# Kernel tuning notes

Measured on AMD Instinct MI355X. Metric: run time of the kernel, lower is better.

Reference implementation:

```python
import jax, jax.numpy as jnp
import numpy as np

N = 50000        # nodes
E = 800000       # edges
F_IN = 128       # num_node_features
H = 128          # hidden_size
C = 128          # num_classes (must be 128 for lin1 to typecheck)
G = 64           # graphs in batch


def setup_inputs() -> dict:
    key = jax.random.key(0)
    ks = jax.random.split(key, 12)
    x = jax.random.normal(ks[0], (N, F_IN), dtype=jnp.float32)
    edge_index = jax.random.randint(ks[1], (2, E), 0, N, dtype=jnp.int64)
    batch = jnp.sort(jax.random.randint(ks[2], (N,), 0, G, dtype=jnp.int64))

    def glorot(k, i, o):
        return jax.random.normal(k, (i, o), dtype=jnp.float32) / np.float32(np.sqrt(i))

    return {
        'x': x, 'edge_index': edge_index, 'batch': batch,
        'W1': glorot(ks[3], F_IN, H), 'b1': jnp.zeros((H,), jnp.float32),
        'W2': glorot(ks[4], H, H),    'b2': jnp.zeros((H,), jnp.float32),
        'W3': glorot(ks[5], H, C),    'b3': jnp.zeros((C,), jnp.float32),
        'Wl': glorot(ks[6], 128, C),  'bl': jnp.zeros((C,), jnp.float32),
    }


def _gcn_conv(x, W, b, src, dst, n):
    # PyG GCNConv: h = x W; out_i = sum_{j->i} d_j^-1/2 d_i^-1/2 h_j + b
    h = x @ W                                                   # [n, out]
    deg = jax.ops.segment_sum(jnp.ones(dst.shape[0], h.dtype), dst, num_segments=n)
    dinv = jnp.where(deg > 0, jax.lax.rsqrt(jnp.maximum(deg, 1.0)), 0.0)
    norm = dinv[src] * dinv[dst]                                # [E+n]
    msg = h[src] * norm[:, None]                                # gather + scale
    return jax.ops.segment_sum(msg, dst, num_segments=n) + b    # scatter-add


def reference(x, edge_index, batch, W1, b1, W2, b2, W3, b3, Wl, bl):
    x = x.astype(jnp.float32)
    loops = jnp.arange(N, dtype=edge_index.dtype)
    src = jnp.concatenate([edge_index[0], loops])  # add self-loops
    dst = jnp.concatenate([edge_index[1], loops])

    h = jax.nn.elu(_gcn_conv(x, W1, b1, src, dst, N))
    h = jax.nn.elu(_gcn_conv(h, W2, b2, src, dst, N))
    h = jax.nn.elu(_gcn_conv(h, W3, b3, src, dst, N))

    # global_mean_pool over batch vector
    cnt = jax.ops.segment_sum(jnp.ones(N, h.dtype), batch, num_segments=G)
    pooled = jax.ops.segment_sum(h, batch, num_segments=G) / jnp.maximum(cnt, 1.0)[:, None]

    # dropout(p=0.2) is identity in eval mode
    return pooled @ Wl + bl
```

## Files before the change

kernel.cpp:

```cpp
#include <hip/hip_runtime.h>
#include <hip/hip_bf16.h>
#include <hip/hip_fp16.h>

#define N_NODES 50000
#define N_GRAPHS 64
#define FILL_CHUNK 4096
#define SLOTS 64
#define SLOT_SHIFT 6
#define PSHIFT 7
#define NPARTS ((N_NODES + 127) >> 7)
#define MM_BLOCKS ((N_NODES + 63) / 64)

typedef _Float16 f16x8 __attribute__((ext_vector_type(8)));
typedef float f32x4 __attribute__((ext_vector_type(4)));


__device__ inline unsigned short f2h_bits(float x) {
    _Float16 h = (_Float16)x;
    return __builtin_bit_cast(unsigned short, h);
}
__device__ inline float h_bits2f(unsigned short b) {
    return (float)__builtin_bit_cast(_Float16, b);
}
__device__ inline unsigned pack_h2(float a, float b) {
    return (unsigned)f2h_bits(a) | ((unsigned)f2h_bits(b) << 16);
}

__device__ inline void fma_h8(float (&acc)[8], uint4 v, float w) {
    acc[0] += w * h_bits2f((unsigned short)(v.x & 0xffffu));
    acc[1] += w * h_bits2f((unsigned short)(v.x >> 16));
    acc[2] += w * h_bits2f((unsigned short)(v.y & 0xffffu));
    acc[3] += w * h_bits2f((unsigned short)(v.y >> 16));
    acc[4] += w * h_bits2f((unsigned short)(v.z & 0xffffu));
    acc[5] += w * h_bits2f((unsigned short)(v.z >> 16));
    acc[6] += w * h_bits2f((unsigned short)(v.w & 0xffffu));
    acc[7] += w * h_bits2f((unsigned short)(v.w >> 16));
}

template<typename BUCKET>
__device__ inline void agg_loop(const uint4* __restrict__ hb4, BUCKET bucket, int n8,
                                int li, float (&acc)[8]) {
    uint4 c0 = make_uint4(0, 0, 0, 0), c1 = c0;
    if (n8 > 0) { c0 = bucket[0]; c1 = bucket[1]; }
    for (int e8 = 0; e8 < n8; ++e8) {
        uint4 nx0 = make_uint4(0, 0, 0, 0), nx1 = nx0;
        if (e8 + 1 < n8) { nx0 = bucket[2 * e8 + 2]; nx1 = bucket[2 * e8 + 3]; }
        uint4 v0 = hb4[(size_t)(c0.x >> 16) * 16 + li];
        uint4 v1 = hb4[(size_t)(c0.y >> 16) * 16 + li];
        uint4 v2 = hb4[(size_t)(c0.z >> 16) * 16 + li];
        uint4 v3 = hb4[(size_t)(c0.w >> 16) * 16 + li];
        uint4 v4 = hb4[(size_t)(c1.x >> 16) * 16 + li];
        uint4 v5 = hb4[(size_t)(c1.y >> 16) * 16 + li];
        uint4 v6 = hb4[(size_t)(c1.z >> 16) * 16 + li];
        uint4 v7 = hb4[(size_t)(c1.w >> 16) * 16 + li];
        fma_h8(acc, v0, h_bits2f((unsigned short)(c0.x & 0xffffu)));
        fma_h8(acc, v1, h_bits2f((unsigned short)(c0.y & 0xffffu)));
        fma_h8(acc, v2, h_bits2f((unsigned short)(c0.z & 0xffffu)));
        fma_h8(acc, v3, h_bits2f((unsigned short)(c0.w & 0xffffu)));
        fma_h8(acc, v4, h_bits2f((unsigned short)(c1.x & 0xffffu)));
        fma_h8(acc, v5, h_bits2f((unsigned short)(c1.y & 0xffffu)));
        fma_h8(acc, v6, h_bits2f((unsigned short)(c1.z & 0xffffu)));
        fma_h8(acc, v7, h_bits2f((unsigned short)(c1.w & 0xffffu)));
        c0 = nx0; c1 = nx1;
    }
}

__device__ inline void bias_elu(const float* __restrict__ bias, float di, int li,
                                float (&acc)[8], float (&o)[8]) {
    float4 b0 = *(const float4*)&bias[li * 8];
    float4 b1 = *(const float4*)&bias[li * 8 + 4];
    o[0] = di * acc[0] + b0.x; o[1] = di * acc[1] + b0.y;
    o[2] = di * acc[2] + b0.z; o[3] = di * acc[3] + b0.w;
    o[4] = di * acc[4] + b1.x; o[5] = di * acc[5] + b1.y;
    o[6] = di * acc[6] + b1.z; o[7] = di * acc[7] + b1.w;
    #pragma unroll
    for (int i = 0; i < 8; ++i) o[i] = o[i] > 0.f ? o[i] : expm1f(o[i]);
}

__device__ inline void aggregate_node(const uint4* __restrict__ hb4,
                                      const int* __restrict__ deg,
                                      const uint4* __restrict__ cvp4,
                                      const float* __restrict__ dinv,
                                      const float* __restrict__ bias,
                                      int node, int li, float (&o)[8]) {
    int dg = min(deg[node], SLOTS);
    int n8 = (dg + 7) >> 3;
    const uint4* bucket = cvp4 + ((size_t)node << (SLOT_SHIFT - 2));
    float di = dinv[node];

    float acc[8];
    #pragma unroll
    for (int i = 0; i < 8; ++i) acc[i] = 0.f;
    uint4 h = hb4[(size_t)node * 16 + li];
    fma_h8(acc, h, di);
    agg_loop(hb4, bucket, n8, li, acc);
    bias_elu(bias, di, li, acc, o);
}


__global__ __launch_bounds__(256) void prep_kernel(const int* __restrict__ dst,
                                                   int* __restrict__ cntmat,
                                                   const float* __restrict__ W1,
                                                   const float* __restrict__ W2,
                                                   const float* __restrict__ W3,
                                                   unsigned short* __restrict__ Wt,
                                                   float* __restrict__ pooled,
                                                   int ne, int nch) {
    int blk = blockIdx.x;
    if (blk < nch) {
        __shared__ int h[NPARTS];
        for (int i = threadIdx.x; i < NPARTS; i += 256) h[i] = 0;
        __syncthreads();
        int beg = blk * FILL_CHUNK, end = min(beg + FILL_CHUNK, ne);
        for (int i = beg + threadIdx.x; i < end; i += 256)
            atomicAdd(&h[dst[i] >> PSHIFT], 1);
        __syncthreads();
        for (int i = threadIdx.x; i < NPARTS; i += 256) cntmat[blk * NPARTS + i] = h[i];
    } else if (blk < nch + 192) {
        int i = (blk - nch) * 256 + threadIdx.x;
        int which = i >> 14;
        const float* W = (which == 0) ? W1 : (which == 1) ? W2 : W3;
        int j = i & 16383;
        int nn = j >> 7, k = j & 127;
        Wt[(which << 14) + nn * 128 + k] = f2h_bits(W[k * 128 + nn]);
    } else {
        int i = (blk - nch - 192) * 256 + threadIdx.x;
        if (i < N_GRAPHS * 128) pooled[i] = 0.f;
    }
}


__global__ __launch_bounds__(256) void scanp_mm_kernel(int* __restrict__ cntmat,
                                                       int* __restrict__ ptotal, int nchunks,
                                                       const float* __restrict__ x,
                                                       const unsigned short* __restrict__ Wt,
                                                       unsigned short* __restrict__ Hh, int n) {
    __shared__ unsigned short Wl[128 * 136];
    int blk = blockIdx.x;
    int t = threadIdx.x;

    if (blk < NPARTS) {
        int* s = (int*)Wl;
        int p = blk;
        int v = (t < nchunks) ? cntmat[t * NPARTS + p] : 0;
        s[t] = v;
        __syncthreads();
        #pragma unroll
        for (int d = 1; d < 256; d <<= 1) {
            int y = (t >= d) ? s[t - d] : 0;
            __syncthreads();
            s[t] += y;
            __syncthreads();
        }
        if (t < nchunks) cntmat[t * NPARTS + p] = s[t] - v;
        if (t == 255) ptotal[p] = s[255];
        return;
    }

    {
        int row = t >> 1, seg = t & 1;
        #pragma unroll
        for (int j = 0; j < 8; ++j) {
            int c = seg * 64 + j * 8;
            *(uint4*)&Wl[row * 136 + c] = *(const uint4*)&Wt[row * 128 + c];
        }
    }
    __syncthreads();

    int w = t >> 6, lane = t & 63;
    int lm = lane & 15, lg = lane >> 4;
    int r0 = (blk - NPARTS) * 64 + w * 16;

    f32x4 acc[8];
    #pragma unroll
    for (int ct = 0; ct < 8; ++ct) acc[ct] = (f32x4){0.f, 0.f, 0.f, 0.f};

    int ar = min(r0 + lm, n - 1);

    #pragma unroll
    for (int kk = 0; kk < 4; ++kk) {
        const float* arow = x + (size_t)ar * 128;
        float4 lo = *(const float4*)&arow[kk * 32 + lg * 8];
        float4 hi = *(const float4*)&arow[kk * 32 + lg * 8 + 4];
        f16x8 a;
        a[0] = (_Float16)lo.x; a[1] = (_Float16)lo.y;
        a[2] = (_Float16)lo.z; a[3] = (_Float16)lo.w;
        a[4] = (_Float16)hi.x; a[5] = (_Float16)hi.y;
        a[6] = (_Float16)hi.z; a[7] = (_Float16)hi.w;
        #pragma unroll
        for (int ct = 0; ct < 8; ++ct) {
            f16x8 b = *(const f16x8*)&Wl[(ct * 16 + lm) * 136 + kk * 32 + lg * 8];
            acc[ct] = __builtin_amdgcn_mfma_f32_16x16x32_f16(a, b, acc[ct], 0, 0, 0);
        }
    }

    #pragma unroll
    for (int ct = 0; ct < 8; ++ct) {
        #pragma unroll
        for (int i = 0; i < 4; ++i) {
            int rr = r0 + lg * 4 + i;
            if (rr < n) Hh[(size_t)rr * 128 + ct * 16 + lm] = f2h_bits(acc[ct][i]);
        }
    }
}

__global__ __launch_bounds__(512) void scant_kernel(const int* __restrict__ ptotal,
                                                    int* __restrict__ pbase) {
    __shared__ int s[512];
    int t = threadIdx.x;
    int v = (t < NPARTS) ? ptotal[t] : 0;
    s[t] = v;
    __syncthreads();
    #pragma unroll
    for (int d = 1; d < 512; d <<= 1) {
        int y = (t >= d) ? s[t - d] : 0;
        __syncthreads();
        s[t] += y;
        __syncthreads();
    }
    if (t < NPARTS) pbase[t] = s[t] - v;
    if (t == NPARTS - 1) pbase[NPARTS] = s[t];
}

__global__ __launch_bounds__(256) void bin_scatter_kernel(const int* __restrict__ src,
                                                          const int* __restrict__ dst,
                                                          const int* __restrict__ cntmat,
                                                          const int* __restrict__ pbase,
                                                          unsigned* __restrict__ binned, int ne) {
    __shared__ int pos[NPARTS];
    int c = blockIdx.x, t = threadIdx.x;
    for (int i = t; i < NPARTS; i += 256) pos[i] = pbase[i] + cntmat[c * NPARTS + i];
    __syncthreads();
    int beg = c * FILL_CHUNK, end = min(beg + FILL_CHUNK, ne);
    for (int i = beg + t; i < end; i += 256) {
        int d = dst[i];
        int p = d >> PSHIFT;
        int idx = atomicAdd(&pos[p], 1);
        binned[idx] = ((unsigned)(d & 127) << 16) | (unsigned)src[i];
    }
}

__global__ __launch_bounds__(256) void bucket_fill_kernel(const unsigned* __restrict__ binned,
                                                          const int* __restrict__ pbase,
                                                          int* __restrict__ deg,
                                                          float* __restrict__ dinv,
                                                          unsigned* __restrict__ tag,
                                                          uint4* __restrict__ cvp4, int n) {
    __shared__ unsigned bkt[128 * SLOTS];
    __shared__ int curls[128];
    int p = blockIdx.x, t = threadIdx.x;
    if (t < 128) curls[t] = 0;
    __syncthreads();
    int beg = pbase[p], end = pbase[p + 1];
    for (int i = beg + t; i < end; i += 256) {
        unsigned e = binned[i];
        int dl = (int)(e >> 16);
        int ps = atomicAdd(&curls[dl], 1);
        if (ps < SLOTS) bkt[(dl << SLOT_SHIFT) + ps] = e & 0xFFFFu;
    }
    __syncthreads();
    int node0 = p << PSHIFT;
    if (t < 128 && node0 + t < n) {
        int c = curls[t];
        deg[node0 + t] = c;
        float dv = rsqrtf((float)c + 1.0f);
        dinv[node0 + t] = dv;
        tag[node0 + t] = ((unsigned)(node0 + t) << 16) | (unsigned)f2h_bits(dv);
    }
    __syncthreads();
    const uint4* b4 = (const uint4*)bkt;
    uint4* outp = cvp4 + (size_t)p * (128 * SLOTS / 4);
    for (int i = t; i < 128 * (SLOTS / 4); i += 256) {
        int r = i >> 4, s4 = i & 15;
        int lim4 = ((min(curls[r], SLOTS) + 7) & ~7) >> 2;
        if (s4 < lim4) outp[i] = b4[i];
    }
}


__global__ __launch_bounds__(256) void fused_tag_agg_mm_kernel(const uint4* __restrict__ hb4,
                                                               const int* __restrict__ deg,
                                                               const unsigned* __restrict__ tag,
                                                               uint4* __restrict__ cvp4,
                                                               const float* __restrict__ dinv,
                                                               const float* __restrict__ bias,
                                                               const unsigned short* __restrict__ Wt,
                                                               unsigned short* __restrict__ Hh,
                                                               int n) {
    __shared__ uint4 bkt4[16 * 16];
    __shared__ unsigned short actl[16 * 136];
    int t = threadIdx.x;
    int nl = t >> 4;
    int li = t & 15;
    int node = blockIdx.x * 16 + nl;

    {
        int slot0 = li << 2;
        int dgn = min(deg[node], SLOTS);
        int lim = (dgn + 7) & ~7;
        uint4 r = make_uint4(0, 0, 0, 0);
        if (slot0 < lim) {
            uint4 v = cvp4[(size_t)node * 16 + li];
            r.x = (slot0     < dgn) ? tag[v.x & 0xFFFFu] : 0u;
            r.y = (slot0 + 1 < dgn) ? tag[v.y & 0xFFFFu] : 0u;
            r.z = (slot0 + 2 < dgn) ? tag[v.z & 0xFFFFu] : 0u;
            r.w = (slot0 + 3 < dgn) ? tag[v.w & 0xFFFFu] : 0u;
            cvp4[(size_t)node * 16 + li] = r;
        }
        bkt4[nl * 16 + li] = r;
    }
    __syncthreads();

    int dg = min(deg[node], SLOTS);
    int n8 = (dg + 7) >> 3;
    float di = dinv[node];

    float acc[8];
    #pragma unroll
    for (int i = 0; i < 8; ++i) acc[i] = 0.f;
    uint4 h = hb4[(size_t)node * 16 + li];
    fma_h8(acc, h, di);
    agg_loop(hb4, (const uint4*)&bkt4[nl * 16], n8, li, acc);

    float o[8];
    bias_elu(bias, di, li, acc, o);

    uint4 pk;
    pk.x = pack_h2(o[0], o[1]);
    pk.y = pack_h2(o[2], o[3]);
    pk.z = pack_h2(o[4], o[5]);
    pk.w = pack_h2(o[6], o[7]);
    *(uint4*)&actl[nl * 136 + li * 8] = pk;

    __syncthreads();

    int w = t >> 6, lane = t & 63;
    int lm = lane & 15, lg = lane >> 4;

    f32x4 macc[2];
    macc[0] = (f32x4){0.f, 0.f, 0.f, 0.f};
    macc[1] = (f32x4){0.f, 0.f, 0.f, 0.f};

    #pragma unroll
    for (int kk = 0; kk < 4; ++kk) {
        f16x8 a = *(const f16x8*)&actl[lm * 136 + kk * 32 + lg * 8];
        #pragma unroll
        for (int j = 0; j < 2; ++j) {
            int ct = w * 2 + j;
            f16x8 b = *(const f16x8*)&Wt[(size_t)(ct * 16 + lm) * 128 + kk * 32 + lg * 8];
            macc[j] = __builtin_amdgcn_mfma_f32_16x16x32_f16(a, b, macc[j], 0, 0, 0);
        }
    }

    #pragma unroll
    for (int j = 0; j < 2; ++j) {
        int ct = w * 2 + j;
        #pragma unroll
        for (int i = 0; i < 4; ++i) {
            int rr = blockIdx.x * 16 + lg * 4 + i;
            Hh[(size_t)rr * 128 + ct * 16 + lm] = f2h_bits(macc[j][i]);
        }
    }
}


__global__ __launch_bounds__(256) void fused_agg_mm_kernel(const uint4* __restrict__ hb4,
                                                           const int* __restrict__ deg,
                                                           const uint4* __restrict__ cvp4,
                                                           const float* __restrict__ dinv,
                                                           const float* __restrict__ bias,
                                                           const unsigned short* __restrict__ Wt,
                                                           unsigned short* __restrict__ Hh,
                                                           int n) {
    __shared__ unsigned short Wl[128 * 136];
    __shared__ unsigned short actl[16 * 136];
    int t = threadIdx.x;

    {
        int row = t >> 1, seg = t & 1;
        #pragma unroll
        for (int j = 0; j < 8; ++j) {
            int c = seg * 64 + j * 8;
            *(uint4*)&Wl[row * 136 + c] = *(const uint4*)&Wt[row * 128 + c];
        }
    }

    int nl = t >> 4;
    int li = t & 15;
    int node = blockIdx.x * 16 + nl;

    float o[8];
    aggregate_node(hb4, deg, cvp4, dinv, bias, node, li, o);

    uint4 pk;
    pk.x = pack_h2(o[0], o[1]);
    pk.y = pack_h2(o[2], o[3]);
    pk.z = pack_h2(o[4], o[5]);
    pk.w = pack_h2(o[6], o[7]);
    *(uint4*)&actl[nl * 136 + li * 8] = pk;

    __syncthreads();

    int w = t >> 6, lane = t & 63;
    int lm = lane & 15, lg = lane >> 4;

    f32x4 macc[2];
    macc[0] = (f32x4){0.f, 0.f, 0.f, 0.f};
    macc[1] = (f32x4){0.f, 0.f, 0.f, 0.f};

    #pragma unroll
    for (int kk = 0; kk < 4; ++kk) {
        f16x8 a = *(const f16x8*)&actl[lm * 136 + kk * 32 + lg * 8];
        #pragma unroll
        for (int j = 0; j < 2; ++j) {
            int ct = w * 2 + j;
            f16x8 b = *(const f16x8*)&Wl[(ct * 16 + lm) * 136 + kk * 32 + lg * 8];
            macc[j] = __builtin_amdgcn_mfma_f32_16x16x32_f16(a, b, macc[j], 0, 0, 0);
        }
    }

    #pragma unroll
    for (int j = 0; j < 2; ++j) {
        int ct = w * 2 + j;
        #pragma unroll
        for (int i = 0; i < 4; ++i) {
            int rr = blockIdx.x * 16 + lg * 4 + i;
            Hh[(size_t)rr * 128 + ct * 16 + lm] = f2h_bits(macc[j][i]);
        }
    }
}


__global__ __launch_bounds__(256) void fused_agg_pool_kernel(const uint4* __restrict__ hb4,
                                                             const int* __restrict__ deg,
                                                             const uint4* __restrict__ cvp4,
                                                             const float* __restrict__ dinv,
                                                             const float* __restrict__ bias,
                                                             const int* __restrict__ batch,
                                                             float* __restrict__ pooled,
                                                             int n) {
    __shared__ float plds[16][132];
    __shared__ int gid[16];
    int t = threadIdx.x;
    int nl = t >> 4;
    int li = t & 15;
    int node = blockIdx.x * 16 + nl;

    if (t < 16) gid[t] = batch[blockIdx.x * 16 + t];

    float o[8];
    aggregate_node(hb4, deg, cvp4, dinv, bias, node, li, o);

    #pragma unroll
    for (int i = 0; i < 8; ++i) plds[nl][li * 8 + i] = o[i];

    __syncthreads();

    int f = t & 127, rg = t >> 7;
    int r0 = rg * 8;
    float local = 0.f;
    int gprev = gid[r0];
    #pragma unroll
    for (int r = r0; r < r0 + 8; ++r) {
        int g = gid[r];
        if (g != gprev) {
            atomicAdd(&pooled[gprev * 128 + f], local);
            local = 0.f;
            gprev = g;
        }
        local += plds[r][f];
    }
    atomicAdd(&pooled[gprev * 128 + f], local);
}


__global__ __launch_bounds__(128) void linear_kernel(const float* __restrict__ pooled,
                                                     const int* __restrict__ batch,
                                                     const float* __restrict__ Wl,
                                                     const float* __restrict__ bl,
                                                     float* __restrict__ out, int n) {
    __shared__ float p[128];
    int g = blockIdx.x, t = threadIdx.x;

    int lo = 0, hi = n;
    while (lo < hi) { int m = (lo + hi) >> 1; if (batch[m] < g) lo = m + 1; else hi = m; }
    int s0 = lo;
    hi = n;
    while (lo < hi) { int m = (lo + hi) >> 1; if (batch[m] < g + 1) lo = m + 1; else hi = m; }
    int e0 = lo;
    float cntf = (float)max(e0 - s0, 1);

    p[t] = pooled[g * 128 + t] / cntf;
    __syncthreads();
    float acc = bl[t];
    for (int k = 0; k < 128; ++k) acc += p[k] * Wl[k * 128 + t];
    out[g * 128 + t] = acc;
}


extern "C" void kernel_launch(void* const* d_in, const int* in_sizes, int n_in,
                              void* d_out, int out_size, void* d_ws, size_t ws_size,
                              hipStream_t stream) {
    const float* x     = (const float*)d_in[0];
    const int*   ei    = (const int*)d_in[1];
    const int*   batch = (const int*)d_in[2];
    const float* W1 = (const float*)d_in[3];
    const float* b1 = (const float*)d_in[4];
    const float* W2 = (const float*)d_in[5];
    const float* b2 = (const float*)d_in[6];
    const float* W3 = (const float*)d_in[7];
    const float* b3 = (const float*)d_in[8];
    const float* Wl = (const float*)d_in[9];
    const float* bl = (const float*)d_in[10];
    float* out = (float*)d_out;

    const int N_ = N_NODES;
    const int E_ = in_sizes[1] / 2;
    const int G_ = N_GRAPHS;
    const int* src = ei;
    const int* dst = ei + E_;
    const int NCH = (E_ + FILL_CHUNK - 1) / FILL_CHUNK;

    char* ws = (char*)d_ws;
    size_t off = 0;
    auto alloc = [&](size_t bytes) -> char* {
        char* p = ws + off;
        off += (bytes + 255) & ~(size_t)255;
        return p;
    };

    float*          dinv   = (float*)          alloc((size_t)N_ * 4);
    unsigned*       tag    = (unsigned*)       alloc((size_t)N_ * 4);
    int*            deg    = (int*)            alloc((size_t)N_ * 4);
    int*            cntmat = (int*)            alloc((size_t)NCH * NPARTS * 4);
    int*            ptotal = (int*)            alloc((size_t)NPARTS * 4);
    int*            pbase  = (int*)            alloc((size_t)(NPARTS + 1) * 4);
    unsigned*       binned = (unsigned*)       alloc((size_t)E_ * 4);
    unsigned*       cvp    = (unsigned*)       alloc((size_t)NPARTS * 128 * SLOTS * 4);
    unsigned short* hbuf   = (unsigned short*) alloc((size_t)N_ * 128 * 2);
    unsigned short* hbuf2  = (unsigned short*) alloc((size_t)N_ * 128 * 2);
    unsigned short* wt     = (unsigned short*) alloc(3 * 128 * 128 * 2);
    float*          pooled = (float*)          alloc((size_t)G_ * 128 * 4);
    (void)ws_size;

    int agblocks = (N_ + 15) / 16;

    prep_kernel<<<NCH + 192 + 32, 256, 0, stream>>>(dst, cntmat, W1, W2, W3, wt, pooled, E_, NCH);
    scanp_mm_kernel<<<NPARTS + MM_BLOCKS, 256, 0, stream>>>(cntmat, ptotal, NCH, x, wt, hbuf, N_);
    scant_kernel<<<1, 512, 0, stream>>>(ptotal, pbase);
    bin_scatter_kernel<<<NCH, 256, 0, stream>>>(src, dst, cntmat, pbase, binned, E_);
    bucket_fill_kernel<<<NPARTS, 256, 0, stream>>>(binned, pbase, deg, dinv, tag, (uint4*)cvp, N_);

    fused_tag_agg_mm_kernel<<<agblocks, 256, 0, stream>>>((const uint4*)hbuf, deg, tag, (uint4*)cvp,
                                                          dinv, b1, wt + 16384, hbuf2, N_);
    fused_agg_mm_kernel<<<agblocks, 256, 0, stream>>>((const uint4*)hbuf2, deg, (const uint4*)cvp,
                                                      dinv, b2, wt + 32768, hbuf, N_);
    fused_agg_pool_kernel<<<agblocks, 256, 0, stream>>>((const uint4*)hbuf, deg, (const uint4*)cvp,
                                                        dinv, b3, batch, pooled, N_);

    linear_kernel<<<G_, 128, 0, stream>>>(pooled, batch, Wl, bl, out, N_);
}
```

Before: 164.2 us.

## Fold partition-total scan into binning kernels and vectorize edge index loads

Removes the single-block scant_kernel launch. Each block of bin_scatter and bucket_fill now recomputes the 512-entry exclusive scan of partition totals itself, using a double-buffered shared-memory scan. The histogram and scatter loops also read dst/src as int4 vectors, four edges per thread, with tail handling. This drops one launch and its serialization point at the cost of redundant scan work and extra shared memory in every block.

```diff
diff --git a/kernel.cpp b/kernel.cpp
--- a/kernel.cpp
+++ b/kernel.cpp
@@ -13,6 +13,7 @@
 
 typedef _Float16 f16x8 __attribute__((ext_vector_type(8)));
 typedef float f32x4 __attribute__((ext_vector_type(4)));
+typedef int i32x4 __attribute__((ext_vector_type(4)));
 
 
 __device__ inline unsigned short f2h_bits(float x) {
@@ -97,6 +98,19 @@
     bias_elu(bias, di, li, acc, o);
 }
 
+__device__ inline int* scan512(int* sA, int* sB, int t) {
+    int* cur = sA; int* nxt = sB;
+    #pragma unroll
+    for (int d = 1; d < 512; d <<= 1) {
+        nxt[t] = cur[t] + ((t >= d) ? cur[t - d] : 0);
+        int k = t + 256;
+        nxt[k] = cur[k] + ((k >= d) ? cur[k - d] : 0);
+        __syncthreads();
+        int* tmp = cur; cur = nxt; nxt = tmp;
+    }
+    return cur;
+}
+
 
 __global__ __launch_bounds__(256) void prep_kernel(const int* __restrict__ dst,
                                                    int* __restrict__ cntmat,
@@ -107,24 +121,42 @@
                                                    float* __restrict__ pooled,
                                                    int ne, int nch) {
     int blk = blockIdx.x;
+    int t = threadIdx.x;
     if (blk < nch) {
         __shared__ int h[NPARTS];
-        for (int i = threadIdx.x; i < NPARTS; i += 256) h[i] = 0;
+        for (int i = t; i < NPARTS; i += 256) h[i] = 0;
         __syncthreads();
         int beg = blk * FILL_CHUNK, end = min(beg + FILL_CHUNK, ne);
-        for (int i = beg + threadIdx.x; i < end; i += 256)
-            atomicAdd(&h[dst[i] >> PSHIFT], 1);
+        for (int i0 = beg + (t << 2); i0 < end; i0 += 1024) {
+            i32x4 d4;
+            if (i0 + 3 < end) {
+                d4 = *(const i32x4*)(dst + i0);
+            } else {
+                d4.x = dst[i0];
+                d4.y = (i0 + 1 < end) ? dst[i0 + 1] : dst[i0];
+                d4.z = (i0 + 2 < end) ? dst[i0 + 2] : dst[i0];
+                d4.w = (i0 + 3 < end) ? dst[i0 + 3] : dst[i0];
+                if (i0 + 1 >= end) d4.y = -1;
+                if (i0 + 2 >= end) d4.z = -1;
+                if (i0 + 3 >= end) d4.w = -1;
+            }
+            #pragma unroll
+            for (int j = 0; j < 4; ++j) {
+                int d = d4[j];
+                if (d >= 0) atomicAdd(&h[d >> PSHIFT], 1);
+            }
+        }
         __syncthreads();
-        for (int i = threadIdx.x; i < NPARTS; i += 256) cntmat[blk * NPARTS + i] = h[i];
+        for (int i = t; i < NPARTS; i += 256) cntmat[blk * NPARTS + i] = h[i];
     } else if (blk < nch + 192) {
-        int i = (blk - nch) * 256 + threadIdx.x;
+        int i = (blk - nch) * 256 + t;
         int which = i >> 14;
         const float* W = (which == 0) ? W1 : (which == 1) ? W2 : W3;
         int j = i & 16383;
         int nn = j >> 7, k = j & 127;
         Wt[(which << 14) + nn * 128 + k] = f2h_bits(W[k * 128 + nn]);
     } else {
-        int i = (blk - nch - 192) * 256 + threadIdx.x;
+        int i = (blk - nch - 192) * 256 + t;
         if (i < N_GRAPHS * 128) pooled[i] = 0.f;
     }
 }
@@ -204,54 +236,73 @@
     }
 }
 
-__global__ __launch_bounds__(512) void scant_kernel(const int* __restrict__ ptotal,
-                                                    int* __restrict__ pbase) {
-    __shared__ int s[512];
-    int t = threadIdx.x;
-    int v = (t < NPARTS) ? ptotal[t] : 0;
-    s[t] = v;
-    __syncthreads();
-    #pragma unroll
-    for (int d = 1; d < 512; d <<= 1) {
-        int y = (t >= d) ? s[t - d] : 0;
-        __syncthreads();
-        s[t] += y;
-        __syncthreads();
-    }
-    if (t < NPARTS) pbase[t] = s[t] - v;
-    if (t == NPARTS - 1) pbase[NPARTS] = s[t];
-}
 
 __global__ __launch_bounds__(256) void bin_scatter_kernel(const int* __restrict__ src,
                                                           const int* __restrict__ dst,
                                                           const int* __restrict__ cntmat,
-                                                          const int* __restrict__ pbase,
+                                                          const int* __restrict__ ptotal,
                                                           unsigned* __restrict__ binned, int ne) {
+    __shared__ int sA[512], sB[512];
     __shared__ int pos[NPARTS];
     int c = blockIdx.x, t = threadIdx.x;
-    for (int i = t; i < NPARTS; i += 256) pos[i] = pbase[i] + cntmat[c * NPARTS + i];
-    __syncthreads();
+
+    int v0 = (t < NPARTS) ? ptotal[t] : 0;
+    int v1 = (t + 256 < NPARTS) ? ptotal[t + 256] : 0;
+    sA[t] = v0;
+    sA[t + 256] = v1;
+    __syncthreads();
+    int* incl = scan512(sA, sB, t);
+
+    if (t < NPARTS) pos[t] = (incl[t] - v0) + cntmat[c * NPARTS + t];
+    if (t + 256 < NPARTS) pos[t + 256] = (incl[t + 256] - v1) + cntmat[c * NPARTS + t + 256];
+    __syncthreads();
+
     int beg = c * FILL_CHUNK, end = min(beg + FILL_CHUNK, ne);
-    for (int i = beg + t; i < end; i += 256) {
-        int d = dst[i];
-        int p = d >> PSHIFT;
-        int idx = atomicAdd(&pos[p], 1);
-        binned[idx] = ((unsigned)(d & 127) << 16) | (unsigned)src[i];
-    }
-}
+    for (int i0 = beg + (t << 2); i0 < end; i0 += 1024) {
+        i32x4 d4, s4;
+        if (i0 + 3 < end) {
+            d4 = *(const i32x4*)(dst + i0);
+            s4 = *(const i32x4*)(src + i0);
+        } else {
+            #pragma unroll
+            for (int j = 0; j < 4; ++j) {
+                d4[j] = (i0 + j < end) ? dst[i0 + j] : -1;
+                s4[j] = (i0 + j < end) ? src[i0 + j] : 0;
+            }
+        }
+        #pragma unroll
+        for (int j = 0; j < 4; ++j) {
+            int d = d4[j];
+            if (d >= 0) {
+                int p = d >> PSHIFT;
+                int idx = atomicAdd(&pos[p], 1);
+                binned[idx] = ((unsigned)(d & 127) << 16) | (unsigned)s4[j];
+            }
+        }
+    }
+}
+
 
 __global__ __launch_bounds__(256) void bucket_fill_kernel(const unsigned* __restrict__ binned,
-                                                          const int* __restrict__ pbase,
+                                                          const int* __restrict__ ptotal,
                                                           int* __restrict__ deg,
                                                           float* __restrict__ dinv,
                                                           unsigned* __restrict__ tag,
                                                           uint4* __restrict__ cvp4, int n) {
     __shared__ unsigned bkt[128 * SLOTS];
     __shared__ int curls[128];
+    __shared__ int sA[512], sB[512];
     int p = blockIdx.x, t = threadIdx.x;
+
+    sA[t] = (t < NPARTS) ? ptotal[t] : 0;
+    sA[t + 256] = (t + 256 < NPARTS) ? ptotal[t + 256] : 0;
     if (t < 128) curls[t] = 0;
     __syncthreads();
-    int beg = pbase[p], end = pbase[p + 1];
+    int* incl = scan512(sA, sB, t);
+    int end = incl[p];
+    int beg = end - ptotal[p];
+    __syncthreads();
+
     for (int i = beg + t; i < end; i += 256) {
         unsigned e = binned[i];
         int dl = (int)(e >> 16);
@@ -534,7 +585,6 @@
     int*            deg    = (int*)            alloc((size_t)N_ * 4);
     int*            cntmat = (int*)            alloc((size_t)NCH * NPARTS * 4);
     int*            ptotal = (int*)            alloc((size_t)NPARTS * 4);
-    int*            pbase  = (int*)            alloc((size_t)(NPARTS + 1) * 4);
     unsigned*       binned = (unsigned*)       alloc((size_t)E_ * 4);
     unsigned*       cvp    = (unsigned*)       alloc((size_t)NPARTS * 128 * SLOTS * 4);
     unsigned short* hbuf   = (unsigned short*) alloc((size_t)N_ * 128 * 2);
@@ -547,9 +597,8 @@
 
     prep_kernel<<<NCH + 192 + 32, 256, 0, stream>>>(dst, cntmat, W1, W2, W3, wt, pooled, E_, NCH);
     scanp_mm_kernel<<<NPARTS + MM_BLOCKS, 256, 0, stream>>>(cntmat, ptotal, NCH, x, wt, hbuf, N_);
-    scant_kernel<<<1, 512, 0, stream>>>(ptotal, pbase);
-    bin_scatter_kernel<<<NCH, 256, 0, stream>>>(src, dst, cntmat, pbase, binned, E_);
-    bucket_fill_kernel<<<NPARTS, 256, 0, stream>>>(binned, pbase, deg, dinv, tag, (uint4*)cvp, N_);
+    bin_scatter_kernel<<<NCH, 256, 0, stream>>>(src, dst, cntmat, ptotal, binned, E_);
+    bucket_fill_kernel<<<NPARTS, 256, 0, stream>>>(binned, ptotal, deg, dinv, tag, (uint4*)cvp, N_);
 
     fused_tag_agg_mm_kernel<<<agblocks, 256, 0, stream>>>((const uint4*)hbuf, deg, tag, (uint4*)cvp,
                                                           dinv, b1, wt + 16384, hbuf2, N_);
```

Result: faster. 157.3 us (-4.2%).
